# Kernel tuning notes

Measured on AMD Instinct MI355X. Metric: run time of the kernel, lower is better.

The kernel has to match this reference:

```python
import jax, jax.numpy as jnp
import numpy as np

B, IN_DIM, R_DIM = 8192, 2048, 4096
LEAK_RATE = 0.3


def setup_inputs() -> dict:
    key = jax.random.key(0)
    k1, k2, k3, k4 = jax.random.split(key, 4)
    inputs = jax.random.normal(k1, (B, IN_DIM), dtype=jnp.float32)
    prev_state = jax.random.normal(k2, (B, R_DIM), dtype=jnp.float32)
    # weights scaled down for numerical sanity inside tanh
    input_weights = jax.random.normal(k3, (R_DIM, IN_DIM), dtype=jnp.float32) * 0.02
    reservoir_weights = jax.random.normal(k4, (R_DIM, R_DIM), dtype=jnp.float32) * 0.02
    return {
        "inputs": inputs,
        "prev_state": prev_state,
        "input_weights": input_weights,
        "reservoir_weights": reservoir_weights,
    }


def reference(inputs, prev_state, input_weights, reservoir_weights):
    # input_part = inputs @ input_weights.T        -> [B, R]
    # reservoir_part = prev_state @ reservoir_weights.T -> [B, R]
    input_part = jnp.einsum("bi,ri->br", inputs, input_weights)
    reservoir_part = jnp.einsum("bq,rq->br", prev_state, reservoir_weights)
    state = (1.0 - LEAK_RATE) * prev_state + LEAK_RATE * jnp.tanh(input_part + reservoir_part)
    return state
```

## Files before the change

### kernel.cpp

```cpp
#include <hip/hip_runtime.h>
#include <cstdint>
#include <cstddef>

typedef unsigned short u16;
typedef __attribute__((ext_vector_type(8))) short short8;
typedef __attribute__((ext_vector_type(16))) float f32x16;
typedef __attribute__((ext_vector_type(4))) int i32x4;

constexpr int M  = 8192;
constexpr int Nn = 4096;
constexpr int K1 = 2048;
constexpr int K2 = 4096;
constexpr int K  = K1 + K2;
constexpr int BM = 256, BN = 256;
constexpr int NKT = K / 64;
constexpr int NBK = K / 64;
constexpr float LEAK = 0.3f;

__device__ __forceinline__ u16 f2bf(float f) {
  unsigned u = __float_as_uint(f);
  u += 0x7FFFu + ((u >> 16) & 1u);
  return (u16)(u >> 16);
}

template<int C1, int C2>
__global__ void cast_concat_blk(const float* __restrict__ X, const float* __restrict__ S,
                                u16* __restrict__ out)
{
  __shared__ u16 tile[64 * 72];
  const int bid = blockIdx.x;
  const int t   = bid % NBK;
  const int g   = bid / NBK;
  const int tid = threadIdx.x;
  const int row = tid >> 2;
  const int cs  = (tid & 3) * 16;
  const int gcol = t * 64 + cs;
  const int grow = g * 64 + row;
  const float* src = (gcol < C1) ? (X + (size_t)grow * C1 + gcol)
                                 : (S + (size_t)grow * C2 + (gcol - C1));
  const float4* s4 = (const float4*)src;
  u16* d = tile + row * 72 + cs;
  #pragma unroll
  for (int q = 0; q < 4; ++q) {
    float4 f = s4[q];
    d[q * 4 + 0] = f2bf(f.x); d[q * 4 + 1] = f2bf(f.y);
    d[q * 4 + 2] = f2bf(f.z); d[q * 4 + 3] = f2bf(f.w);
  }
  __syncthreads();
  u16* ob = out + (size_t)bid * 4096;
  #pragma unroll
  for (int h = 0; h < 2; ++h) {
    const int s   = tid + h * 256;
    const int rb2 = s >> 8, kc = (s >> 5) & 7, r = s & 31;
    const u16* p  = tile + (rb2 * 32 + r) * 72 + kc * 8;
    *(i32x4*)(ob + s * 8) = *(const i32x4*)p;
  }
}

__device__ __forceinline__ void gload16(const u16* g, u16* l) {
  __builtin_amdgcn_global_load_lds(
      (const __attribute__((address_space(1))) void*)g,
      (__attribute__((address_space(3))) void*)l, 16, 0, 0);
}

__device__ __forceinline__ float fast_tanh(float x) {
  const float ax = __builtin_fabsf(x);
  const float e  = __builtin_amdgcn_exp2f(ax * 2.8853900817779268f);
  const float r  = 1.0f - 2.0f * __builtin_amdgcn_rcpf(e + 1.0f);
  return __builtin_copysignf(r, x);
}

#define BAR()   __builtin_amdgcn_s_barrier()
#define LGKM0() asm volatile("s_waitcnt lgkmcnt(0)" ::: "memory")
#define LGKM4() asm volatile("s_waitcnt lgkmcnt(4)" ::: "memory")
#define LGKM8() asm volatile("s_waitcnt lgkmcnt(8)" ::: "memory")
#define VMW8()  asm volatile("s_waitcnt vmcnt(8)" ::: "memory")
#define VMW0()  asm volatile("s_waitcnt vmcnt(0)" ::: "memory")
#define SB0()   __builtin_amdgcn_sched_barrier(0)

__global__ __launch_bounds__(512, 2) void gemm_fused(
    const u16* __restrict__ A,
    const u16* __restrict__ W,
    const float* __restrict__ prev,
    float* __restrict__ out)
{
  __shared__ u16 lds[65536];

  const int tid  = threadIdx.x;
  const int lane = tid & 63;
  const int wid  = tid >> 6;
  const int wr   = wid >> 2;
  const int wc   = wid & 3;

  const int cpx = gridDim.x >> 3;
  const int wg  = ((int)blockIdx.x & 7) * cpx + ((int)blockIdx.x >> 3);
  const int bn  = wg & 15;
  const int bm  = wg >> 4;

  constexpr size_t BLK = 4096;
  constexpr size_t RG  = (size_t)NBK * BLK;
  const u16* pA = A + (size_t)(4 * bm) * RG + tid * 8;
  const u16* pW = W + (size_t)(4 * bn) * RG + tid * 8;
  u16* ldsw = lds + wid * 512;

  auto stg = [&](const u16* g, int dst) {
    gload16(g,      ldsw + dst);
    gload16(g + RG, ldsw + dst + 4096);
  };

  short8 afE[2][4], afO[2][4];
  short8 bfE[4],    bfO[4];
  f32x16 acc[4][2];
  #pragma unroll
  for (int mt = 0; mt < 4; ++mt)
    #pragma unroll
    for (int ng = 0; ng < 2; ++ng) acc[mt][ng] = (f32x16)0.f;

  auto dsA = [&](short8 (&Av)[2][4], int mg, int ab) {
    #pragma unroll
    for (int mtl = 0; mtl < 2; ++mtl) {
      const int rb = wr * 4 + mg * 2 + mtl;
      #pragma unroll
      for (int ks = 0; ks < 4; ++ks)
        Av[mtl][ks] = *(const short8*)(lds + ab + rb * 2048 + ks * 512 + lane * 8);
    }
  };
  auto dsB = [&](short8 (&Bv)[4], int ng, int bb) {
    const int rb = wc * 2 + ng;
    #pragma unroll
    for (int ks = 0; ks < 4; ++ks)
      Bv[ks] = *(const short8*)(lds + bb + rb * 2048 + ks * 512 + lane * 8);
  };
  auto MM = [&](short8 (&Av)[2][4], short8 (&Bv)[4], int mg, int ng) {
    __builtin_amdgcn_s_setprio(1);
    #pragma unroll
    for (int ks = 0; ks < 4; ++ks)
      #pragma unroll
      for (int mtl = 0; mtl < 2; ++mtl)
        acc[mg * 2 + mtl][ng] = __builtin_amdgcn_mfma_f32_32x32x16_bf16(
            Av[mtl][ks], Bv[ks], acc[mg * 2 + mtl][ng], 0, 0, 0);
    __builtin_amdgcn_s_setprio(0);
  };

  stg(pW,                32768); stg(pW + 2 * RG,       32768 + 8192);
  stg(pA,                0);     stg(pA + 2 * RG,       8192);
  stg(pW + BLK,          49152); stg(pW + 2 * RG + BLK, 49152 + 8192);
  stg(pA + BLK,          16384); stg(pA + 2 * RG + BLK, 16384 + 8192);
  VMW8();
  BAR();
  dsA(afE, 0, 0);
  dsB(bfE, 0, 32768);

  const u16* gA = pA;
  const u16* gW = pW;
  #pragma unroll 1
  for (int i = 0; i < 47; ++i) {
    dsB(bfO, 1, 32768);
    LGKM4(); SB0(); MM(afE, bfE, 0, 0); BAR();
    dsA(afO, 1, 0);
    LGKM8(); SB0(); MM(afE, bfO, 0, 1); VMW0(); BAR();
    dsA(afE, 0, 16384);
    stg(gW + 2 * BLK, 32768); stg(gW + 2 * RG + 2 * BLK, 32768 + 8192);
    LGKM8(); SB0(); MM(afO, bfE, 1, 0); BAR();
    dsB(bfE, 0, 49152);
    stg(gA + 2 * BLK, 0); stg(gA + 2 * RG + 2 * BLK, 8192);
    SB0(); MM(afO, bfO, 1, 1); BAR();
    dsB(bfO, 1, 49152);
    LGKM4(); SB0(); MM(afE, bfE, 0, 0); BAR();
    dsA(afO, 1, 16384);
    LGKM8(); SB0(); MM(afE, bfO, 0, 1); VMW0(); BAR();
    dsA(afE, 0, 0);
    stg(gW + 3 * BLK, 49152); stg(gW + 2 * RG + 3 * BLK, 49152 + 8192);
    LGKM8(); SB0(); MM(afO, bfE, 1, 0); BAR();
    dsB(bfE, 0, 32768);
    stg(gA + 3 * BLK, 16384); stg(gA + 2 * RG + 3 * BLK, 16384 + 8192);
    SB0(); MM(afO, bfO, 1, 1); BAR();
    gA += 2 * BLK; gW += 2 * BLK;
  }

  dsB(bfO, 1, 32768);
  LGKM4(); SB0(); MM(afE, bfE, 0, 0); BAR();
  dsA(afO, 1, 0);
  LGKM8(); SB0(); MM(afE, bfO, 0, 1); VMW0(); BAR();
  dsA(afE, 0, 16384);
  LGKM8(); SB0(); MM(afO, bfE, 1, 0); BAR();
  dsB(bfE, 0, 49152);
  SB0(); MM(afO, bfO, 1, 1); BAR();
  dsB(bfO, 1, 49152);
  LGKM4(); SB0(); MM(afE, bfE, 0, 0); BAR();
  dsA(afO, 1, 16384);
  LGKM8(); SB0(); MM(afE, bfO, 0, 1); BAR();
  LGKM0(); SB0(); MM(afO, bfE, 1, 0);
  MM(afO, bfO, 1, 1);

  const int l31 = lane & 31, l5 = lane >> 5;
  const int crow0 = bm * BM + wr * 128 + l5 * 4;
  const int ccol0 = bn * BN + wc * 64 + l31;
  #pragma unroll
  for (int mt = 0; mt < 4; ++mt)
    #pragma unroll
    for (int ng = 0; ng < 2; ++ng)
      #pragma unroll
      for (int j = 0; j < 16; ++j) {
        const int row = crow0 + mt * 32 + (j & 3) + 8 * (j >> 2);
        const size_t off = (size_t)row * Nn + ccol0 + ng * 32;
        out[off] = (1.0f - LEAK) * prev[off] + LEAK * fast_tanh(acc[mt][ng][j]);
      }
}

extern "C" void kernel_launch(void* const* d_in, const int* in_sizes, int n_in,
                              void* d_out, int out_size, void* d_ws, size_t ws_size,
                              hipStream_t stream) {
  const float* inputs = (const float*)d_in[0];
  const float* prev   = (const float*)d_in[1];
  const float* w_in   = (const float*)d_in[2];
  const float* w_res  = (const float*)d_in[3];
  float* out = (float*)d_out;

  u16* Acat = (u16*)d_ws;
  u16* Wcat = Acat + (size_t)M * K;

  cast_concat_blk<K1, K2><<<(M / 64) * NBK, 256, 0, stream>>>(inputs, prev, Acat);
  cast_concat_blk<K1, K2><<<(Nn / 64) * NBK, 256, 0, stream>>>(w_in, w_res, Wcat);

  gemm_fused<<<(M / BM) * (Nn / BN), 512, 0, stream>>>(Acat, Wcat, prev, out);
}
```

Measured before the change: 449.9 us.

## Load A fragments directly from global into registers, stage only B in LDS

The A operand is no longer staged through LDS. Each wave loads its A fragments straight from global memory into registers, which is possible because the cast kernel already writes A in the pre-blocked fragment layout. Only W tiles are double-buffered in LDS, halving shared memory and LDS read traffic, with the vmcnt waits reworked to match. The cost is higher global load latency on the MFMA critical path, and A is now fetched redundantly by the four waves that share each row group.

```diff
diff --git a/kernel.cpp b/kernel.cpp
--- a/kernel.cpp
+++ b/kernel.cpp
@@ -13,7 +13,6 @@
 constexpr int K2 = 4096;
 constexpr int K  = K1 + K2;
 constexpr int BM = 256, BN = 256;
-constexpr int NKT = K / 64;
 constexpr int NBK = K / 64;
 constexpr float LEAK = 0.3f;
 
@@ -70,13 +69,13 @@
   return __builtin_copysignf(r, x);
 }
 
-#define BAR()   __builtin_amdgcn_s_barrier()
-#define LGKM0() asm volatile("s_waitcnt lgkmcnt(0)" ::: "memory")
-#define LGKM4() asm volatile("s_waitcnt lgkmcnt(4)" ::: "memory")
-#define LGKM8() asm volatile("s_waitcnt lgkmcnt(8)" ::: "memory")
-#define VMW8()  asm volatile("s_waitcnt vmcnt(8)" ::: "memory")
-#define VMW0()  asm volatile("s_waitcnt vmcnt(0)" ::: "memory")
-#define SB0()   __builtin_amdgcn_sched_barrier(0)
+#define BAR()    __builtin_amdgcn_s_barrier()
+#define LGKM0()  asm volatile("s_waitcnt lgkmcnt(0)" ::: "memory")
+#define LGKM4()  asm volatile("s_waitcnt lgkmcnt(4)" ::: "memory")
+#define VMW4()   asm volatile("s_waitcnt vmcnt(4)" ::: "memory")
+#define VMW8()   asm volatile("s_waitcnt vmcnt(8)" ::: "memory")
+#define VMW12()  asm volatile("s_waitcnt vmcnt(12)" ::: "memory")
+#define SB0()    __builtin_amdgcn_sched_barrier(0)
 
 __global__ __launch_bounds__(512, 2) void gemm_fused(
     const u16* __restrict__ A,
@@ -84,7 +83,7 @@
     const float* __restrict__ prev,
     float* __restrict__ out)
 {
-  __shared__ u16 lds[65536];
+  __shared__ u16 lds[32768];
 
   const int tid  = threadIdx.x;
   const int lane = tid & 63;
@@ -98,14 +97,13 @@
   const int bm  = wg >> 4;
 
   constexpr size_t BLK = 4096;
-  constexpr size_t RG  = (size_t)NBK * BLK;
-  const u16* pA = A + (size_t)(4 * bm) * RG + tid * 8;
-  const u16* pW = W + (size_t)(4 * bn) * RG + tid * 8;
   u16* ldsw = lds + wid * 512;
 
-  auto stg = [&](const u16* g, int dst) {
-    gload16(g,      ldsw + dst);
-    gload16(g + RG, ldsw + dst + 4096);
+  auto stgB = [&](int t, int bufel) {
+    #pragma unroll
+    for (int r = 0; r < 4; ++r)
+      gload16(W + ((size_t)(4 * bn + r) * NBK + t) * BLK + tid * 8,
+              ldsw + bufel + r * 4096);
   };
 
   short8 afE[2][4], afO[2][4];
@@ -116,14 +114,13 @@
     #pragma unroll
     for (int ng = 0; ng < 2; ++ng) acc[mt][ng] = (f32x16)0.f;
 
-  auto dsA = [&](short8 (&Av)[2][4], int mg, int ab) {
-    #pragma unroll
-    for (int mtl = 0; mtl < 2; ++mtl) {
-      const int rb = wr * 4 + mg * 2 + mtl;
+  auto gldA = [&](short8 (&Av)[2][4], int mg, int t) {
+    const u16* g = A + ((size_t)(4 * bm + wr * 2 + mg) * NBK + t) * BLK + lane * 8;
+    #pragma unroll
+    for (int mtl = 0; mtl < 2; ++mtl)
       #pragma unroll
       for (int ks = 0; ks < 4; ++ks)
-        Av[mtl][ks] = *(const short8*)(lds + ab + rb * 2048 + ks * 512 + lane * 8);
-    }
+        Av[mtl][ks] = *(const short8*)(g + mtl * 2048 + ks * 512);
   };
   auto dsB = [&](short8 (&Bv)[4], int ng, int bb) {
     const int rb = wc * 2 + ng;
@@ -142,55 +139,53 @@
     __builtin_amdgcn_s_setprio(0);
   };
 
-  stg(pW,                32768); stg(pW + 2 * RG,       32768 + 8192);
-  stg(pA,                0);     stg(pA + 2 * RG,       8192);
-  stg(pW + BLK,          49152); stg(pW + 2 * RG + BLK, 49152 + 8192);
-  stg(pA + BLK,          16384); stg(pA + 2 * RG + BLK, 16384 + 8192);
-  VMW8();
+  gldA(afE, 0, 0);
+  SB0();
+  stgB(0, 0);
+  stgB(1, 16384);
+  VMW4();
   BAR();
-  dsA(afE, 0, 0);
-  dsB(bfE, 0, 32768);
-
-  const u16* gA = pA;
-  const u16* gW = pW;
+  dsB(bfE, 0, 0);
+
   #pragma unroll 1
   for (int i = 0; i < 47; ++i) {
-    dsB(bfO, 1, 32768);
+    const int T = 2 * i;
+    dsB(bfO, 1, 0);
     LGKM4(); SB0(); MM(afE, bfE, 0, 0); BAR();
-    dsA(afO, 1, 0);
-    LGKM8(); SB0(); MM(afE, bfO, 0, 1); VMW0(); BAR();
-    dsA(afE, 0, 16384);
-    stg(gW + 2 * BLK, 32768); stg(gW + 2 * RG + 2 * BLK, 32768 + 8192);
-    LGKM8(); SB0(); MM(afO, bfE, 1, 0); BAR();
-    dsB(bfE, 0, 49152);
-    stg(gA + 2 * BLK, 0); stg(gA + 2 * RG + 2 * BLK, 8192);
+    gldA(afO, 1, T);
+    LGKM0(); SB0(); MM(afE, bfO, 0, 1); BAR();
+    gldA(afE, 0, T + 1);
+    SB0();
+    stgB(T + 2, 0);
+    VMW12(); SB0(); MM(afO, bfE, 1, 0); BAR();
+    dsB(bfE, 0, 16384);
     SB0(); MM(afO, bfO, 1, 1); BAR();
-    dsB(bfO, 1, 49152);
+    dsB(bfO, 1, 16384);
     LGKM4(); SB0(); MM(afE, bfE, 0, 0); BAR();
-    dsA(afO, 1, 16384);
-    LGKM8(); SB0(); MM(afE, bfO, 0, 1); VMW0(); BAR();
-    dsA(afE, 0, 0);
-    stg(gW + 3 * BLK, 49152); stg(gW + 2 * RG + 3 * BLK, 49152 + 8192);
-    LGKM8(); SB0(); MM(afO, bfE, 1, 0); BAR();
-    dsB(bfE, 0, 32768);
-    stg(gA + 3 * BLK, 16384); stg(gA + 2 * RG + 3 * BLK, 16384 + 8192);
+    gldA(afO, 1, T + 1);
+    LGKM0(); SB0(); MM(afE, bfO, 0, 1); BAR();
+    gldA(afE, 0, T + 2);
+    SB0();
+    stgB(T + 3, 16384);
+    VMW12(); SB0(); MM(afO, bfE, 1, 0); BAR();
+    dsB(bfE, 0, 0);
     SB0(); MM(afO, bfO, 1, 1); BAR();
-    gA += 2 * BLK; gW += 2 * BLK;
   }
 
-  dsB(bfO, 1, 32768);
+  dsB(bfO, 1, 0);
   LGKM4(); SB0(); MM(afE, bfE, 0, 0); BAR();
-  dsA(afO, 1, 0);
-  LGKM8(); SB0(); MM(afE, bfO, 0, 1); VMW0(); BAR();
-  dsA(afE, 0, 16384);
-  LGKM8(); SB0(); MM(afO, bfE, 1, 0); BAR();
-  dsB(bfE, 0, 49152);
+  gldA(afO, 1, 94);
+  LGKM0(); SB0(); MM(afE, bfO, 0, 1); BAR();
+  gldA(afE, 0, 95);
+  VMW8();
+  SB0(); MM(afO, bfE, 1, 0); BAR();
+  dsB(bfE, 0, 16384);
   SB0(); MM(afO, bfO, 1, 1); BAR();
-  dsB(bfO, 1, 49152);
+  dsB(bfO, 1, 16384);
   LGKM4(); SB0(); MM(afE, bfE, 0, 0); BAR();
-  dsA(afO, 1, 16384);
-  LGKM8(); SB0(); MM(afE, bfO, 0, 1); BAR();
-  LGKM0(); SB0(); MM(afO, bfE, 1, 0);
+  gldA(afO, 1, 95);
+  LGKM0(); SB0(); MM(afE, bfO, 0, 1); BAR();
+  SB0(); MM(afO, bfE, 1, 0);
   MM(afO, bfO, 1, 1);
 
   const int l31 = lane & 31, l5 = lane >> 5;
```

After: 614.0 us. +36.5%, slower.
